# Kernel tuning notes

Hardware: AMD Instinct MI355X
Metric: run time of the kernel (lower is better)

Reference implementation:

```python
import jax, jax.numpy as jnp
import numpy as np

N_NODES = 100000
N_EDGES = 1600000
F_IN = 128
HID = 128
N_CLS = 40


def _glorot(key, shape):
    fan_in, fan_out = shape[0], shape[1]
    lim = (6.0 / (fan_in + fan_out)) ** 0.5
    return jax.random.uniform(key, shape, jnp.float32, -lim, lim)


def setup_inputs() -> dict:
    key = jax.random.key(0)
    ks = jax.random.split(key, 10)
    x = jax.random.normal(ks[0], (N_NODES, F_IN), jnp.float32)
    edge_index = jax.random.randint(ks[1], (2, N_EDGES), 0, N_NODES, jnp.int64)
    return {
        "x": x,
        "edge_index": edge_index,
        "W1l": _glorot(ks[2], (F_IN, HID)),   # applied to aggregated neighbors
        "W1r": _glorot(ks[3], (F_IN, HID)),   # applied to root features
        "b1": jnp.zeros((HID,), jnp.float32),
        "W2l": _glorot(ks[4], (HID, HID)),
        "W2r": _glorot(ks[5], (HID, HID)),
        "b2": jnp.zeros((HID,), jnp.float32),
        "Wout": _glorot(ks[6], (HID, N_CLS)),
        "bout": jnp.zeros((N_CLS,), jnp.float32),
    }


def _sage_conv(x, src, dst, Wl, Wr, b):
    # mean aggregation of neighbor messages x[src] at dst, then linear combine
    msgs = x[src]                                                   # [E, F] gather
    agg = jax.ops.segment_sum(msgs, dst, num_segments=N_NODES)      # [N, F]
    cnt = jax.ops.segment_sum(jnp.ones((src.shape[0],), x.dtype), dst,
                              num_segments=N_NODES)                 # [N]
    agg = agg / jnp.maximum(cnt, 1.0)[:, None]
    return agg @ Wl + x @ Wr + b


def reference(x, edge_index, W1l, W1r, b1, W2l, W2r, b2, Wout, bout):
    src, dst = edge_index[0], edge_index[1]
    h = jax.nn.relu(_sage_conv(x, src, dst, W1l, W1r, b1))
    # dropout is identity in deterministic (eval) reference
    h = jax.nn.relu(_sage_conv(h, src, dst, W2l, W2r, b2))
    return h @ Wout + bout
```

## Files before the change

### kernel.cpp

```cpp
#include <hip/hip_runtime.h>
#include <hip/hip_bf16.h>

#define N_NODES 100000
#define N_EDGES 1600000
#define FDIM 128
#define NCLS 40
#define NCLS_PAD 48

#define NBINS ((N_NODES + 255) / 256)
#define NBLKB 128
#define CHUNKB (N_EDGES / NBLKB)
#define SCANTOT (NBINS * NBLKB)
#define SCANB_NB ((SCANTOT + 1023) / 1024)

typedef __attribute__((ext_vector_type(8))) short short8;
typedef __attribute__((ext_vector_type(4))) float f32x4;

__device__ __forceinline__ float bf2f(unsigned short u) {
    union { unsigned int i; float f; } v; v.i = ((unsigned int)u) << 16; return v.f;
}
__device__ __forceinline__ unsigned short f2bf(float f) {
    __hip_bfloat16 h = __float2bfloat16(f);
    return *reinterpret_cast<unsigned short*>(&h);
}

__global__ void k_cvt_bf16(const float4* __restrict__ in, ushort4* __restrict__ out, int n4) {
    int i = blockIdx.x * blockDim.x + threadIdx.x;
    if (i >= n4) return;
    float4 v = in[i];
    ushort4 o;
    o.x = f2bf(v.x); o.y = f2bf(v.y); o.z = f2bf(v.z); o.w = f2bf(v.w);
    out[i] = o;
}

__global__ __launch_bounds__(256) void k_countB(const int* __restrict__ dst, int* __restrict__ bh) {
    __shared__ unsigned h[NBINS];
    for (int r = threadIdx.x; r < NBINS; r += 256) h[r] = 0u;
    __syncthreads();
    int base = blockIdx.x * CHUNKB;
    int end = base + CHUNKB; if (end > N_EDGES) end = N_EDGES;
    for (int e = base + threadIdx.x; e < end; e += 256)
        atomicAdd(&h[dst[e] >> 8], 1u);
    __syncthreads();
    for (int r = threadIdx.x; r < NBINS; r += 256)
        bh[blockIdx.x * NBINS + r] = (int)h[r];
}

__global__ __launch_bounds__(1024) void k_scanB1(const int* __restrict__ bh,
                                                 int* __restrict__ obh,
                                                 unsigned* __restrict__ bsumB) {
    __shared__ unsigned lds[1024];
    int t = threadIdx.x;
    int g = blockIdx.x * 1024 + t;
    unsigned v = 0u;
    int r = g >> 7, b = g & (NBLKB - 1);
    if (g < SCANTOT) v = (unsigned)bh[b * NBINS + r];
    lds[t] = v;
    __syncthreads();
    for (int d = 1; d < 1024; d <<= 1) {
        unsigned add = (t >= d) ? lds[t - d] : 0u;
        __syncthreads();
        lds[t] += add;
        __syncthreads();
    }
    if (g < SCANTOT) obh[b * NBINS + r] = (int)(lds[t] - v);
    if (t == 1023) bsumB[blockIdx.x] = lds[t];
}

__global__ void k_scanB2(const unsigned* __restrict__ bsumB, unsigned* __restrict__ boffB) {
    __shared__ unsigned lds[64];
    int t = threadIdx.x;
    unsigned v = (t < SCANB_NB) ? bsumB[t] : 0u;
    lds[t] = v;
    __syncthreads();
    for (int d = 1; d < 64; d <<= 1) {
        unsigned add = (t >= d) ? lds[t - d] : 0u;
        __syncthreads();
        lds[t] += add;
        __syncthreads();
    }
    if (t < SCANB_NB) boffB[t] = lds[t] - v;
}

__global__ __launch_bounds__(1024) void k_scanB3(int* __restrict__ obh,
                                                 const unsigned* __restrict__ boffB,
                                                 int* __restrict__ bucketbase) {
    int t = threadIdx.x;
    int g = blockIdx.x * 1024 + t;
    if (g < SCANTOT) {
        int r = g >> 7, b = g & (NBLKB - 1);
        int val = obh[b * NBINS + r] + (int)boffB[blockIdx.x];
        obh[b * NBINS + r] = val;
        if (b == 0) bucketbase[r] = val;
    }
    if (g == 0) bucketbase[NBINS] = N_EDGES;
}

__global__ __launch_bounds__(256) void k_binwriteB(const int* __restrict__ src, const int* __restrict__ dst,
                                                   const int* __restrict__ obh,
                                                   unsigned long long* __restrict__ bpack) {
    __shared__ unsigned pos[NBINS];
    for (int r = threadIdx.x; r < NBINS; r += 256)
        pos[r] = (unsigned)obh[blockIdx.x * NBINS + r];
    __syncthreads();
    int base = blockIdx.x * CHUNKB;
    int end = base + CHUNKB; if (end > N_EDGES) end = N_EDGES;
    for (int e = base + threadIdx.x; e < end; e += 256) {
        int d = dst[e];
        unsigned p = atomicAdd(&pos[d >> 8], 1u);
        bpack[p] = ((unsigned long long)(unsigned)d << 32) | (unsigned)src[e];
    }
}

__global__ __launch_bounds__(256) void k_bucket_csr(const unsigned long long* __restrict__ bpack,
                                                    const int* __restrict__ bucketbase,
                                                    int* __restrict__ rowptr,
                                                    int* __restrict__ esrc) {
    __shared__ unsigned c[256];
    int b = blockIdx.x;
    int t = threadIdx.x;
    int bb = bucketbase[b], be = bucketbase[b + 1];
    c[t] = 0u;
    __syncthreads();
    for (int i = bb + t; i < be; i += 256)
        atomicAdd(&c[(unsigned)(bpack[i] >> 32) & 255u], 1u);
    __syncthreads();
    unsigned own = c[t];
    for (int d = 1; d < 256; d <<= 1) {
        unsigned add = (t >= d) ? c[t - d] : 0u;
        __syncthreads();
        c[t] += add;
        __syncthreads();
    }
    unsigned excl = c[t] - own;
    int node = (b << 8) + t;
    if (node < N_NODES) rowptr[node] = bb + (int)excl;
    if (b == NBINS - 1 && t == 0) rowptr[N_NODES] = N_EDGES;
    __syncthreads();
    c[t] = excl;
    __syncthreads();
    for (int i = bb + t; i < be; i += 256) {
        unsigned long long p = bpack[i];
        unsigned slot = atomicAdd(&c[(unsigned)(p >> 32) & 255u], 1u);
        esrc[bb + (int)slot] = (int)(unsigned)p;
    }
}

__global__ void k_aggregate(const unsigned short* __restrict__ feat,
                            const int* __restrict__ esrc,
                            const int* __restrict__ rowptr,
                            unsigned short* __restrict__ out) {
    int node = blockIdx.x * 4 + (threadIdx.x >> 6);
    if (node >= N_NODES) return;
    int lane = threadIdx.x & 63;
    int sub = lane >> 4;
    int fl = lane & 15;
    int s = rowptr[node], e = rowptr[node + 1];
    float acc[8];
#pragma unroll
    for (int q = 0; q < 8; ++q) acc[q] = 0.f;

    for (int j = s + sub; j < e; j += 4) {
        int sv = esrc[j];
        short8 v = *(const short8*)(feat + (size_t)sv * FDIM + fl * 8);
#pragma unroll
        for (int q = 0; q < 8; ++q) acc[q] += bf2f((unsigned short)v[q]);
    }
#pragma unroll
    for (int q = 0; q < 8; ++q) {
        acc[q] += __shfl_xor(acc[q], 16, 64);
        acc[q] += __shfl_xor(acc[q], 32, 64);
    }
    int deg = e - s;
    float inv = 1.0f / (float)(deg > 1 ? deg : 1);
    if (sub == 0) {
        short8 o;
#pragma unroll
        for (int q = 0; q < 8; ++q) o[q] = (short)f2bf(acc[q] * inv);
        *(short8*)(out + (size_t)node * FDIM + fl * 8) = o;
    }
}

__global__ void k_pack(const float* __restrict__ Wl, const float* __restrict__ Wr,
                       const float* __restrict__ bin, unsigned short* __restrict__ Bp,
                       float* __restrict__ bout, int ncols_out, int ncols_src, int Keach) {
    int K = (Wr != nullptr) ? 2 * Keach : Keach;
    int idx = blockIdx.x * blockDim.x + threadIdx.x;
    if (idx >= ncols_out * K) return;
    int col = idx / K, k = idx % K;
    float v = 0.f;
    if (col < ncols_src)
        v = (k < Keach) ? Wl[(size_t)k * ncols_src + col]
                        : Wr[(size_t)(k - Keach) * ncols_src + col];
    Bp[((size_t)(k >> 3) * ncols_out + col) * 8 + (k & 7)] = f2bf(v);
    if (k == 0) bout[col] = (col < ncols_src) ? bin[col] : 0.f;
}

__global__ __launch_bounds__(256) void k_gemm_layer(
        const unsigned short* __restrict__ A0, const unsigned short* __restrict__ A1,
        const unsigned short* __restrict__ Bp, const float* __restrict__ bias,
        unsigned short* __restrict__ out) {
    int wave = threadIdx.x >> 6;
    int lane = threadIdx.x & 63;
    int rowblk = blockIdx.x * 64 + wave * 16;
    int lrow = lane & 15;
    int kgrp = lane >> 4;
    int arow = rowblk + lrow; if (arow > N_NODES - 1) arow = N_NODES - 1;

    f32x4 acc[8];
#pragma unroll
    for (int c = 0; c < 8; ++c) acc[c] = (f32x4){0.f, 0.f, 0.f, 0.f};

#pragma unroll
    for (int kb = 0; kb < 8; ++kb) {
        const unsigned short* Asrc = (kb < 4) ? A0 : A1;
        int kk = (kb & 3) * 32 + kgrp * 8;
        short8 a = *(const short8*)(Asrc + (size_t)arow * FDIM + kk);
        int k8 = kb * 4 + kgrp;
        const unsigned short* brow = Bp + ((size_t)k8 * FDIM + lrow) * 8;
#pragma unroll
        for (int c = 0; c < 8; ++c) {
            short8 b = *(const short8*)(brow + c * 16 * 8);
            acc[c] = __builtin_amdgcn_mfma_f32_16x16x32_bf16(a, b, acc[c], 0, 0, 0);
        }
    }

    int orowbase = rowblk + kgrp * 4;
#pragma unroll
    for (int c = 0; c < 8; ++c) {
        int col = c * 16 + lrow;
        float bv = bias[col];
#pragma unroll
        for (int i = 0; i < 4; ++i) {
            int r = orowbase + i;
            if (r < N_NODES) {
                float v = acc[c][i] + bv;
                v = fmaxf(v, 0.f);
                out[(size_t)r * FDIM + col] = f2bf(v);
            }
        }
    }
}

__global__ __launch_bounds__(256) void k_gemm_out(
        const unsigned short* __restrict__ A0, const unsigned short* __restrict__ Bp,
        const float* __restrict__ bias, float* __restrict__ out) {
    int wave = threadIdx.x >> 6;
    int lane = threadIdx.x & 63;
    int rowblk = blockIdx.x * 64 + wave * 16;
    int lrow = lane & 15;
    int kgrp = lane >> 4;
    int arow = rowblk + lrow; if (arow > N_NODES - 1) arow = N_NODES - 1;

    f32x4 acc[3];
#pragma unroll
    for (int c = 0; c < 3; ++c) acc[c] = (f32x4){0.f, 0.f, 0.f, 0.f};

#pragma unroll
    for (int kb = 0; kb < 4; ++kb) {
        int kk = kb * 32 + kgrp * 8;
        short8 a = *(const short8*)(A0 + (size_t)arow * FDIM + kk);
        int k8 = kb * 4 + kgrp;
        const unsigned short* brow = Bp + ((size_t)k8 * NCLS_PAD + lrow) * 8;
#pragma unroll
        for (int c = 0; c < 3; ++c) {
            short8 b = *(const short8*)(brow + c * 16 * 8);
            acc[c] = __builtin_amdgcn_mfma_f32_16x16x32_bf16(a, b, acc[c], 0, 0, 0);
        }
    }

    int orowbase = rowblk + kgrp * 4;
#pragma unroll
    for (int c = 0; c < 3; ++c) {
        int col = c * 16 + lrow;
        if (col < NCLS) {
            float bv = bias[col];
#pragma unroll
            for (int i = 0; i < 4; ++i) {
                int r = orowbase + i;
                if (r < N_NODES)
                    out[(size_t)r * NCLS + col] = acc[c][i] + bv;
            }
        }
    }
}

extern "C" void kernel_launch(void* const* d_in, const int* in_sizes, int n_in,
                              void* d_out, int out_size, void* d_ws, size_t ws_size,
                              hipStream_t stream) {
    const float* x    = (const float*)d_in[0];
    const int*   ei   = (const int*)d_in[1];
    const float* W1l  = (const float*)d_in[2];
    const float* W1r  = (const float*)d_in[3];
    const float* b1   = (const float*)d_in[4];
    const float* W2l  = (const float*)d_in[5];
    const float* W2r  = (const float*)d_in[6];
    const float* b2   = (const float*)d_in[7];
    const float* Wout = (const float*)d_in[8];
    const float* bout = (const float*)d_in[9];
    const int* src = ei;
    const int* dst = ei + N_EDGES;

    char* ws = (char*)d_ws;
    size_t off = 0;
    auto alloc = [&](size_t bytes) -> void* {
        void* p = ws + off;
        off += (bytes + 255) & ~(size_t)255;
        return p;
    };
    unsigned short* xb   = (unsigned short*)alloc((size_t)N_NODES * FDIM * 2);
    unsigned short* aggn = (unsigned short*)alloc((size_t)N_NODES * FDIM * 2);
    unsigned short* h1   = (unsigned short*)alloc((size_t)N_NODES * FDIM * 2);
    unsigned short* h2   = (unsigned short*)alloc((size_t)N_NODES * FDIM * 2);
    unsigned short* Bp1  = (unsigned short*)alloc((size_t)FDIM * 256 * 2);
    unsigned short* Bp2  = (unsigned short*)alloc((size_t)FDIM * 256 * 2);
    unsigned short* Bp3  = (unsigned short*)alloc((size_t)NCLS_PAD * FDIM * 2);
    float* b1p = (float*)alloc(FDIM * 4);
    float* b2p = (float*)alloc(FDIM * 4);
    float* b3p = (float*)alloc(NCLS_PAD * 4);
    int* rowptr    = (int*)alloc((size_t)(N_NODES + 1) * 4);
    int* esrc      = (int*)alloc((size_t)N_EDGES * 4);
    int* bh        = (int*)alloc((size_t)NBLKB * NBINS * 4);
    int* obh       = (int*)alloc((size_t)NBLKB * NBINS * 4);
    int* bucketbase= (int*)alloc((size_t)(NBINS + 1) * 4);
    unsigned* bsumB = (unsigned*)alloc((size_t)SCANB_NB * 4);
    unsigned* boffB = (unsigned*)alloc((size_t)SCANB_NB * 4);
    unsigned long long* bpack = (unsigned long long*)alloc((size_t)N_EDGES * 8);

    int n4 = N_NODES * FDIM / 4;
    k_cvt_bf16<<<(n4 + 255) / 256, 256, 0, stream>>>((const float4*)x, (ushort4*)xb, n4);

    k_pack<<<(FDIM * 256 + 255) / 256, 256, 0, stream>>>(W1l, W1r, b1, Bp1, b1p, FDIM, FDIM, FDIM);
    k_pack<<<(FDIM * 256 + 255) / 256, 256, 0, stream>>>(W2l, W2r, b2, Bp2, b2p, FDIM, FDIM, FDIM);
    k_pack<<<(NCLS_PAD * FDIM + 255) / 256, 256, 0, stream>>>(Wout, nullptr, bout, Bp3, b3p, NCLS_PAD, NCLS, FDIM);

    k_countB<<<NBLKB, 256, 0, stream>>>(dst, bh);
    k_scanB1<<<SCANB_NB, 1024, 0, stream>>>(bh, obh, bsumB);
    k_scanB2<<<1, 64, 0, stream>>>(bsumB, boffB);
    k_scanB3<<<SCANB_NB, 1024, 0, stream>>>(obh, boffB, bucketbase);
    k_binwriteB<<<NBLKB, 256, 0, stream>>>(src, dst, obh, bpack);
    k_bucket_csr<<<NBINS, 256, 0, stream>>>(bpack, bucketbase, rowptr, esrc);

    int aggGrid = (N_NODES + 3) / 4;
    int gemmGrid = (N_NODES + 63) / 64;

    k_aggregate<<<aggGrid, 256, 0, stream>>>(xb, esrc, rowptr, aggn);
    k_gemm_layer<<<gemmGrid, 256, 0, stream>>>(aggn, xb, Bp1, b1p, h1);
    k_aggregate<<<aggGrid, 256, 0, stream>>>(h1, esrc, rowptr, aggn);
    k_gemm_layer<<<gemmGrid, 256, 0, stream>>>(aggn, h1, Bp2, b2p, h2);
    k_gemm_out<<<gemmGrid, 256, 0, stream>>>(h2, Bp3, b3p, (float*)d_out);
}
```

Before: 293.1 us.

## Fuse neighbor aggregation into the layer GEMMs via LDS and merge the pack kernels

Each wave now gathers and mean-aggregates its 16 nodes into an LDS tile, then runs the MFMA GEMM directly from LDS. This removes the aggn intermediate round-trip through global memory. The second layer also keeps its ReLU output in LDS and applies the output projection in the same kernel, removing the h2 buffer. The three weight-pack launches are merged into one. The tradeoff is less gather parallelism: there are now 1563 blocks, each looping serially over 16 nodes per wave, instead of 25000 small blocks. That can reduce latency hiding for the irregular gathers.

```diff
diff --git a/kernel.cpp b/kernel.cpp
--- a/kernel.cpp
+++ b/kernel.cpp
@@ -12,6 +12,8 @@
 #define CHUNKB (N_EDGES / NBLKB)
 #define SCANTOT (NBINS * NBLKB)
 #define SCANB_NB ((SCANTOT + 1023) / 1024)
+
+#define LPAD 136
 
 typedef __attribute__((ext_vector_type(8))) short short8;
 typedef __attribute__((ext_vector_type(4))) float f32x4;
@@ -146,47 +148,10 @@
     }
 }
 
-__global__ void k_aggregate(const unsigned short* __restrict__ feat,
-                            const int* __restrict__ esrc,
-                            const int* __restrict__ rowptr,
-                            unsigned short* __restrict__ out) {
-    int node = blockIdx.x * 4 + (threadIdx.x >> 6);
-    if (node >= N_NODES) return;
-    int lane = threadIdx.x & 63;
-    int sub = lane >> 4;
-    int fl = lane & 15;
-    int s = rowptr[node], e = rowptr[node + 1];
-    float acc[8];
-#pragma unroll
-    for (int q = 0; q < 8; ++q) acc[q] = 0.f;
-
-    for (int j = s + sub; j < e; j += 4) {
-        int sv = esrc[j];
-        short8 v = *(const short8*)(feat + (size_t)sv * FDIM + fl * 8);
-#pragma unroll
-        for (int q = 0; q < 8; ++q) acc[q] += bf2f((unsigned short)v[q]);
-    }
-#pragma unroll
-    for (int q = 0; q < 8; ++q) {
-        acc[q] += __shfl_xor(acc[q], 16, 64);
-        acc[q] += __shfl_xor(acc[q], 32, 64);
-    }
-    int deg = e - s;
-    float inv = 1.0f / (float)(deg > 1 ? deg : 1);
-    if (sub == 0) {
-        short8 o;
-#pragma unroll
-        for (int q = 0; q < 8; ++q) o[q] = (short)f2bf(acc[q] * inv);
-        *(short8*)(out + (size_t)node * FDIM + fl * 8) = o;
-    }
-}
-
-__global__ void k_pack(const float* __restrict__ Wl, const float* __restrict__ Wr,
-                       const float* __restrict__ bin, unsigned short* __restrict__ Bp,
-                       float* __restrict__ bout, int ncols_out, int ncols_src, int Keach) {
+__device__ __forceinline__ void pack_one(const float* Wl, const float* Wr, const float* bin,
+                                         unsigned short* Bp, float* bout,
+                                         int ncols_out, int ncols_src, int Keach, int idx) {
     int K = (Wr != nullptr) ? 2 * Keach : Keach;
-    int idx = blockIdx.x * blockDim.x + threadIdx.x;
-    if (idx >= ncols_out * K) return;
     int col = idx / K, k = idx % K;
     float v = 0.f;
     if (col < ncols_src)
@@ -196,36 +161,84 @@
     if (k == 0) bout[col] = (col < ncols_src) ? bin[col] : 0.f;
 }
 
-__global__ __launch_bounds__(256) void k_gemm_layer(
-        const unsigned short* __restrict__ A0, const unsigned short* __restrict__ A1,
+#define PACK1 (FDIM * 256)
+#define PACK2 (FDIM * 256)
+#define PACK3 (NCLS_PAD * FDIM)
+__global__ void k_pack_all(const float* __restrict__ W1l, const float* __restrict__ W1r,
+                           const float* __restrict__ b1, unsigned short* __restrict__ Bp1, float* __restrict__ b1p,
+                           const float* __restrict__ W2l, const float* __restrict__ W2r,
+                           const float* __restrict__ b2, unsigned short* __restrict__ Bp2, float* __restrict__ b2p,
+                           const float* __restrict__ Wout, const float* __restrict__ bo,
+                           unsigned short* __restrict__ Bp3, float* __restrict__ b3p) {
+    int idx = blockIdx.x * blockDim.x + threadIdx.x;
+    if (idx < PACK1) { pack_one(W1l, W1r, b1, Bp1, b1p, FDIM, FDIM, FDIM, idx); return; }
+    idx -= PACK1;
+    if (idx < PACK2) { pack_one(W2l, W2r, b2, Bp2, b2p, FDIM, FDIM, FDIM, idx); return; }
+    idx -= PACK2;
+    if (idx < PACK3) { pack_one(Wout, nullptr, bo, Bp3, b3p, NCLS_PAD, NCLS, FDIM, idx); }
+}
+
+__global__ __launch_bounds__(256) void k_fused_layer(
+        const unsigned short* __restrict__ feat,
+        const int* __restrict__ esrc, const int* __restrict__ rowptr,
         const unsigned short* __restrict__ Bp, const float* __restrict__ bias,
         unsigned short* __restrict__ out) {
-    int wave = threadIdx.x >> 6;
-    int lane = threadIdx.x & 63;
-    int rowblk = blockIdx.x * 64 + wave * 16;
-    int lrow = lane & 15;
-    int kgrp = lane >> 4;
-    int arow = rowblk + lrow; if (arow > N_NODES - 1) arow = N_NODES - 1;
-
-    f32x4 acc[8];
-#pragma unroll
-    for (int c = 0; c < 8; ++c) acc[c] = (f32x4){0.f, 0.f, 0.f, 0.f};
+    __shared__ unsigned short Alds[4][16][LPAD];
+    int wave = threadIdx.x >> 6, lane = threadIdx.x & 63;
+    int sub = lane >> 4, fl = lane & 15;
+    int wbase = blockIdx.x * 64 + wave * 16;
+
+    for (int n = 0; n < 16; ++n) {
+        int node = wbase + n;
+        float acc[8];
+#pragma unroll
+        for (int q = 0; q < 8; ++q) acc[q] = 0.f;
+        int deg = 0;
+        if (node < N_NODES) {
+            int s = rowptr[node], e = rowptr[node + 1];
+            deg = e - s;
+            for (int j = s + sub; j < e; j += 4) {
+                int sv = esrc[j];
+                short8 v = *(const short8*)(feat + (size_t)sv * FDIM + fl * 8);
+#pragma unroll
+                for (int q = 0; q < 8; ++q) acc[q] += bf2f((unsigned short)v[q]);
+            }
+        }
+#pragma unroll
+        for (int q = 0; q < 8; ++q) {
+            acc[q] += __shfl_xor(acc[q], 16, 64);
+            acc[q] += __shfl_xor(acc[q], 32, 64);
+        }
+        if (sub == 0) {
+            float inv = 1.0f / (float)(deg > 1 ? deg : 1);
+            short8 o;
+#pragma unroll
+            for (int q = 0; q < 8; ++q) o[q] = (short)f2bf(acc[q] * inv);
+            *(short8*)(&Alds[wave][n][fl * 8]) = o;
+        }
+    }
+
+    int lrow = lane & 15, kgrp = lane >> 4;
+    int arow = wbase + lrow; if (arow > N_NODES - 1) arow = N_NODES - 1;
+    f32x4 acc2[8];
+#pragma unroll
+    for (int c = 0; c < 8; ++c) acc2[c] = (f32x4){0.f, 0.f, 0.f, 0.f};
 
 #pragma unroll
     for (int kb = 0; kb < 8; ++kb) {
-        const unsigned short* Asrc = (kb < 4) ? A0 : A1;
-        int kk = (kb & 3) * 32 + kgrp * 8;
-        short8 a = *(const short8*)(Asrc + (size_t)arow * FDIM + kk);
+        short8 a;
+        if (kb < 4) a = *(const short8*)(&Alds[wave][lrow][kb * 32 + kgrp * 8]);
+        else        a = *(const short8*)(feat + (size_t)arow * FDIM + (kb - 4) * 32 + kgrp * 8);
         int k8 = kb * 4 + kgrp;
         const unsigned short* brow = Bp + ((size_t)k8 * FDIM + lrow) * 8;
 #pragma unroll
         for (int c = 0; c < 8; ++c) {
             short8 b = *(const short8*)(brow + c * 16 * 8);
-            acc[c] = __builtin_amdgcn_mfma_f32_16x16x32_bf16(a, b, acc[c], 0, 0, 0);
-        }
-    }
-
-    int orowbase = rowblk + kgrp * 4;
+            acc2[c] = __builtin_amdgcn_mfma_f32_16x16x32_bf16(a, b, acc2[c], 0, 0, 0);
+        }
+    }
+
+    int orowbase = wbase + kgrp * 4;
 #pragma unroll
     for (int c = 0; c < 8; ++c) {
         int col = c * 16 + lrow;
@@ -234,7 +247,7 @@
         for (int i = 0; i < 4; ++i) {
             int r = orowbase + i;
             if (r < N_NODES) {
-                float v = acc[c][i] + bv;
+                float v = acc2[c][i] + bv;
                 v = fmaxf(v, 0.f);
                 out[(size_t)r * FDIM + col] = f2bf(v);
             }
@@ -242,44 +255,107 @@
     }
 }
 
-__global__ __launch_bounds__(256) void k_gemm_out(
-        const unsigned short* __restrict__ A0, const unsigned short* __restrict__ Bp,
-        const float* __restrict__ bias, float* __restrict__ out) {
-    int wave = threadIdx.x >> 6;
-    int lane = threadIdx.x & 63;
-    int rowblk = blockIdx.x * 64 + wave * 16;
-    int lrow = lane & 15;
-    int kgrp = lane >> 4;
-    int arow = rowblk + lrow; if (arow > N_NODES - 1) arow = N_NODES - 1;
-
-    f32x4 acc[3];
-#pragma unroll
-    for (int c = 0; c < 3; ++c) acc[c] = (f32x4){0.f, 0.f, 0.f, 0.f};
+__global__ __launch_bounds__(256) void k_fused_final(
+        const unsigned short* __restrict__ feat,
+        const int* __restrict__ esrc, const int* __restrict__ rowptr,
+        const unsigned short* __restrict__ Bp, const float* __restrict__ bias,
+        const unsigned short* __restrict__ Bp3, const float* __restrict__ bias3,
+        float* __restrict__ out) {
+    __shared__ unsigned short Alds[4][16][LPAD];
+    int wave = threadIdx.x >> 6, lane = threadIdx.x & 63;
+    int sub = lane >> 4, fl = lane & 15;
+    int wbase = blockIdx.x * 64 + wave * 16;
+
+    for (int n = 0; n < 16; ++n) {
+        int node = wbase + n;
+        float acc[8];
+#pragma unroll
+        for (int q = 0; q < 8; ++q) acc[q] = 0.f;
+        int deg = 0;
+        if (node < N_NODES) {
+            int s = rowptr[node], e = rowptr[node + 1];
+            deg = e - s;
+            for (int j = s + sub; j < e; j += 4) {
+                int sv = esrc[j];
+                short8 v = *(const short8*)(feat + (size_t)sv * FDIM + fl * 8);
+#pragma unroll
+                for (int q = 0; q < 8; ++q) acc[q] += bf2f((unsigned short)v[q]);
+            }
+        }
+#pragma unroll
+        for (int q = 0; q < 8; ++q) {
+            acc[q] += __shfl_xor(acc[q], 16, 64);
+            acc[q] += __shfl_xor(acc[q], 32, 64);
+        }
+        if (sub == 0) {
+            float inv = 1.0f / (float)(deg > 1 ? deg : 1);
+            short8 o;
+#pragma unroll
+            for (int q = 0; q < 8; ++q) o[q] = (short)f2bf(acc[q] * inv);
+            *(short8*)(&Alds[wave][n][fl * 8]) = o;
+        }
+    }
+
+    int lrow = lane & 15, kgrp = lane >> 4;
+    int arow = wbase + lrow; if (arow > N_NODES - 1) arow = N_NODES - 1;
+    f32x4 acc2[8];
+#pragma unroll
+    for (int c = 0; c < 8; ++c) acc2[c] = (f32x4){0.f, 0.f, 0.f, 0.f};
+
+#pragma unroll
+    for (int kb = 0; kb < 8; ++kb) {
+        short8 a;
+        if (kb < 4) a = *(const short8*)(&Alds[wave][lrow][kb * 32 + kgrp * 8]);
+        else        a = *(const short8*)(feat + (size_t)arow * FDIM + (kb - 4) * 32 + kgrp * 8);
+        int k8 = kb * 4 + kgrp;
+        const unsigned short* brow = Bp + ((size_t)k8 * FDIM + lrow) * 8;
+#pragma unroll
+        for (int c = 0; c < 8; ++c) {
+            short8 b = *(const short8*)(brow + c * 16 * 8);
+            acc2[c] = __builtin_amdgcn_mfma_f32_16x16x32_bf16(a, b, acc2[c], 0, 0, 0);
+        }
+    }
+
+    int srowbase = kgrp * 4;
+#pragma unroll
+    for (int c = 0; c < 8; ++c) {
+        int col = c * 16 + lrow;
+        float bv = bias[col];
+#pragma unroll
+        for (int i = 0; i < 4; ++i) {
+            float v = acc2[c][i] + bv;
+            v = fmaxf(v, 0.f);
+            Alds[wave][srowbase + i][col] = f2bf(v);
+        }
+    }
+
+    f32x4 acc3[3];
+#pragma unroll
+    for (int c = 0; c < 3; ++c) acc3[c] = (f32x4){0.f, 0.f, 0.f, 0.f};
 
 #pragma unroll
     for (int kb = 0; kb < 4; ++kb) {
-        int kk = kb * 32 + kgrp * 8;
-        short8 a = *(const short8*)(A0 + (size_t)arow * FDIM + kk);
+        short8 a = *(const short8*)(&Alds[wave][lrow][kb * 32 + kgrp * 8]);
         int k8 = kb * 4 + kgrp;
-        const unsigned short* brow = Bp + ((size_t)k8 * NCLS_PAD + lrow) * 8;
+        const unsigned short* brow = Bp3 + ((size_t)k8 * NCLS_PAD + lrow) * 8;
 #pragma unroll
         for (int c = 0; c < 3; ++c) {
             short8 b = *(const short8*)(brow + c * 16 * 8);
-            acc[c] = __builtin_amdgcn_mfma_f32_16x16x32_bf16(a, b, acc[c], 0, 0, 0);
-        }
-    }
-
-    int orowbase = rowblk + kgrp * 4;
+            acc3[c] = __builtin_amdgcn_mfma_f32_16x16x32_bf16(a, b, acc3[c], 0, 0, 0);
+        }
+    }
+
+    int orowbase = wbase + kgrp * 4;
 #pragma unroll
     for (int c = 0; c < 3; ++c) {
         int col = c * 16 + lrow;
         if (col < NCLS) {
-            float bv = bias[col];
+            float bv = bias3[col];
 #pragma unroll
             for (int i = 0; i < 4; ++i) {
                 int r = orowbase + i;
                 if (r < N_NODES)
-                    out[(size_t)r * NCLS + col] = acc[c][i] + bv;
+                    out[(size_t)r * NCLS + col] = acc3[c][i] + bv;
             }
         }
     }
@@ -309,9 +385,7 @@
         return p;
     };
     unsigned short* xb   = (unsigned short*)alloc((size_t)N_NODES * FDIM * 2);
-    unsigned short* aggn = (unsigned short*)alloc((size_t)N_NODES * FDIM * 2);
     unsigned short* h1   = (unsigned short*)alloc((size_t)N_NODES * FDIM * 2);
-    unsigned short* h2   = (unsigned short*)alloc((size_t)N_NODES * FDIM * 2);
     unsigned short* Bp1  = (unsigned short*)alloc((size_t)FDIM * 256 * 2);
     unsigned short* Bp2  = (unsigned short*)alloc((size_t)FDIM * 256 * 2);
     unsigned short* Bp3  = (unsigned short*)alloc((size_t)NCLS_PAD * FDIM * 2);
@@ -330,9 +404,9 @@
     int n4 = N_NODES * FDIM / 4;
     k_cvt_bf16<<<(n4 + 255) / 256, 256, 0, stream>>>((const float4*)x, (ushort4*)xb, n4);
 
-    k_pack<<<(FDIM * 256 + 255) / 256, 256, 0, stream>>>(W1l, W1r, b1, Bp1, b1p, FDIM, FDIM, FDIM);
-    k_pack<<<(FDIM * 256 + 255) / 256, 256, 0, stream>>>(W2l, W2r, b2, Bp2, b2p, FDIM, FDIM, FDIM);
-    k_pack<<<(NCLS_PAD * FDIM + 255) / 256, 256, 0, stream>>>(Wout, nullptr, bout, Bp3, b3p, NCLS_PAD, NCLS, FDIM);
+    int packTot = PACK1 + PACK2 + PACK3;
+    k_pack_all<<<(packTot + 255) / 256, 256, 0, stream>>>(
+        W1l, W1r, b1, Bp1, b1p, W2l, W2r, b2, Bp2, b2p, Wout, bout, Bp3, b3p);
 
     k_countB<<<NBLKB, 256, 0, stream>>>(dst, bh);
     k_scanB1<<<SCANB_NB, 1024, 0, stream>>>(bh, obh, bsumB);
@@ -341,12 +415,8 @@
     k_binwriteB<<<NBLKB, 256, 0, stream>>>(src, dst, obh, bpack);
     k_bucket_csr<<<NBINS, 256, 0, stream>>>(bpack, bucketbase, rowptr, esrc);
 
-    int aggGrid = (N_NODES + 3) / 4;
-    int gemmGrid = (N_NODES + 63) / 64;
-
-    k_aggregate<<<aggGrid, 256, 0, stream>>>(xb, esrc, rowptr, aggn);
-    k_gemm_layer<<<gemmGrid, 256, 0, stream>>>(aggn, xb, Bp1, b1p, h1);
-    k_aggregate<<<aggGrid, 256, 0, stream>>>(h1, esrc, rowptr, aggn);
-    k_gemm_layer<<<gemmGrid, 256, 0, stream>>>(aggn, h1, Bp2, b2p, h2);
-    k_gemm_out<<<gemmGrid, 256, 0, stream>>>(h2, Bp3, b3p, (float*)d_out);
-}
+    int fusedGrid = (N_NODES + 63) / 64;
+
+    k_fused_layer<<<fusedGrid, 256, 0, stream>>>(xb, esrc, rowptr, Bp1, b1p, h1);
+    k_fused_final<<<fusedGrid, 256, 0, stream>>>(h1, esrc, rowptr, Bp2, b2p, Bp3, b3p, (float*)d_out);
+}
```

New measurement: 353.3 us. 1.21x slower.

## Fuse prologue kernels, merge scan passes, fuse layer-2 GEMM with output GEMM

Applied to the files above, without the earlier changes.

Combines the edge-count, bf16 conversion and weight-pack kernels into one prologue launch with block-range dispatch. It folds the small block-offset scan into the final scan pass. It also fuses the second SAGE layer GEMM with the classifier GEMM by staging the ReLU'd bf16 tile in LDS per wave. This avoids writing and re-reading the h2 intermediate and cuts several launches. The cost is more LDS use and some redundant serial scan work per block.

```diff
diff --git a/kernel.cpp b/kernel.cpp
--- a/kernel.cpp
+++ b/kernel.cpp
@@ -13,6 +13,16 @@
 #define SCANTOT (NBINS * NBLKB)
 #define SCANB_NB ((SCANTOT + 1023) / 1024)
 
+#define LPAD 136
+
+#define PACK1 (FDIM * 256)
+#define PACK2 (FDIM * 256)
+#define PACK3 (NCLS_PAD * FDIM)
+#define PACKTOT (PACK1 + PACK2 + PACK3)
+#define PACK_NB ((PACKTOT + 255) / 256)
+#define CVT_N4 (N_NODES * FDIM / 4)
+#define CVT_NB ((CVT_N4 + 255) / 256)
+
 typedef __attribute__((ext_vector_type(8))) short short8;
 typedef __attribute__((ext_vector_type(4))) float f32x4;
 
@@ -24,26 +34,60 @@
     return *reinterpret_cast<unsigned short*>(&h);
 }
 
-__global__ void k_cvt_bf16(const float4* __restrict__ in, ushort4* __restrict__ out, int n4) {
-    int i = blockIdx.x * blockDim.x + threadIdx.x;
-    if (i >= n4) return;
-    float4 v = in[i];
-    ushort4 o;
-    o.x = f2bf(v.x); o.y = f2bf(v.y); o.z = f2bf(v.z); o.w = f2bf(v.w);
-    out[i] = o;
-}
-
-__global__ __launch_bounds__(256) void k_countB(const int* __restrict__ dst, int* __restrict__ bh) {
+__device__ __forceinline__ void pack_one(const float* Wl, const float* Wr, const float* bin,
+                                         unsigned short* Bp, float* bout,
+                                         int ncols_out, int ncols_src, int Keach, int idx) {
+    int K = (Wr != nullptr) ? 2 * Keach : Keach;
+    int col = idx / K, k = idx % K;
+    float v = 0.f;
+    if (col < ncols_src)
+        v = (k < Keach) ? Wl[(size_t)k * ncols_src + col]
+                        : Wr[(size_t)(k - Keach) * ncols_src + col];
+    Bp[((size_t)(k >> 3) * ncols_out + col) * 8 + (k & 7)] = f2bf(v);
+    if (k == 0) bout[col] = (col < ncols_src) ? bin[col] : 0.f;
+}
+
+__global__ __launch_bounds__(256) void k_prologue(
+        const int* __restrict__ dst, int* __restrict__ bh,
+        const float4* __restrict__ x4, ushort4* __restrict__ xb4,
+        const float* __restrict__ W1l, const float* __restrict__ W1r,
+        const float* __restrict__ b1, unsigned short* __restrict__ Bp1, float* __restrict__ b1p,
+        const float* __restrict__ W2l, const float* __restrict__ W2r,
+        const float* __restrict__ b2, unsigned short* __restrict__ Bp2, float* __restrict__ b2p,
+        const float* __restrict__ Wout, const float* __restrict__ bo,
+        unsigned short* __restrict__ Bp3, float* __restrict__ b3p) {
     __shared__ unsigned h[NBINS];
-    for (int r = threadIdx.x; r < NBINS; r += 256) h[r] = 0u;
-    __syncthreads();
-    int base = blockIdx.x * CHUNKB;
-    int end = base + CHUNKB; if (end > N_EDGES) end = N_EDGES;
-    for (int e = base + threadIdx.x; e < end; e += 256)
-        atomicAdd(&h[dst[e] >> 8], 1u);
-    __syncthreads();
-    for (int r = threadIdx.x; r < NBINS; r += 256)
-        bh[blockIdx.x * NBINS + r] = (int)h[r];
+    int b = blockIdx.x;
+    if (b < NBLKB) {
+        for (int r = threadIdx.x; r < NBINS; r += 256) h[r] = 0u;
+        __syncthreads();
+        int base = b * CHUNKB;
+        int end = base + CHUNKB; if (end > N_EDGES) end = N_EDGES;
+        for (int e = base + threadIdx.x; e < end; e += 256)
+            atomicAdd(&h[dst[e] >> 8], 1u);
+        __syncthreads();
+        for (int r = threadIdx.x; r < NBINS; r += 256)
+            bh[b * NBINS + r] = (int)h[r];
+        return;
+    }
+    b -= NBLKB;
+    if (b < CVT_NB) {
+        int i = b * 256 + threadIdx.x;
+        if (i < CVT_N4) {
+            float4 v = x4[i];
+            ushort4 o;
+            o.x = f2bf(v.x); o.y = f2bf(v.y); o.z = f2bf(v.z); o.w = f2bf(v.w);
+            xb4[i] = o;
+        }
+        return;
+    }
+    b -= CVT_NB;
+    int idx = b * 256 + threadIdx.x;
+    if (idx < PACK1) { pack_one(W1l, W1r, b1, Bp1, b1p, FDIM, FDIM, FDIM, idx); return; }
+    idx -= PACK1;
+    if (idx < PACK2) { pack_one(W2l, W2r, b2, Bp2, b2p, FDIM, FDIM, FDIM, idx); return; }
+    idx -= PACK2;
+    if (idx < PACK3) { pack_one(Wout, nullptr, bo, Bp3, b3p, NCLS_PAD, NCLS, FDIM, idx); }
 }
 
 __global__ __launch_bounds__(1024) void k_scanB1(const int* __restrict__ bh,
@@ -67,29 +111,22 @@
     if (t == 1023) bsumB[blockIdx.x] = lds[t];
 }
 
-__global__ void k_scanB2(const unsigned* __restrict__ bsumB, unsigned* __restrict__ boffB) {
-    __shared__ unsigned lds[64];
+__global__ __launch_bounds__(1024) void k_scanB3(int* __restrict__ obh,
+                                                 const unsigned* __restrict__ bsumB,
+                                                 int* __restrict__ bucketbase) {
+    __shared__ unsigned soff[SCANB_NB];
     int t = threadIdx.x;
-    unsigned v = (t < SCANB_NB) ? bsumB[t] : 0u;
-    lds[t] = v;
-    __syncthreads();
-    for (int d = 1; d < 64; d <<= 1) {
-        unsigned add = (t >= d) ? lds[t - d] : 0u;
-        __syncthreads();
-        lds[t] += add;
-        __syncthreads();
-    }
-    if (t < SCANB_NB) boffB[t] = lds[t] - v;
-}
-
-__global__ __launch_bounds__(1024) void k_scanB3(int* __restrict__ obh,
-                                                 const unsigned* __restrict__ boffB,
-                                                 int* __restrict__ bucketbase) {
-    int t = threadIdx.x;
+    if (t < SCANB_NB) soff[t] = bsumB[t];
+    __syncthreads();
+    if (t == 0) {
+        unsigned run = 0;
+        for (int i = 0; i < SCANB_NB; ++i) { unsigned v = soff[i]; soff[i] = run; run += v; }
+    }
+    __syncthreads();
     int g = blockIdx.x * 1024 + t;
     if (g < SCANTOT) {
         int r = g >> 7, b = g & (NBLKB - 1);
-        int val = obh[b * NBINS + r] + (int)boffB[blockIdx.x];
+        int val = obh[b * NBINS + r] + (int)soff[blockIdx.x];
         obh[b * NBINS + r] = val;
         if (b == 0) bucketbase[r] = val;
     }
@@ -181,21 +218,6 @@
     }
 }
 
-__global__ void k_pack(const float* __restrict__ Wl, const float* __restrict__ Wr,
-                       const float* __restrict__ bin, unsigned short* __restrict__ Bp,
-                       float* __restrict__ bout, int ncols_out, int ncols_src, int Keach) {
-    int K = (Wr != nullptr) ? 2 * Keach : Keach;
-    int idx = blockIdx.x * blockDim.x + threadIdx.x;
-    if (idx >= ncols_out * K) return;
-    int col = idx / K, k = idx % K;
-    float v = 0.f;
-    if (col < ncols_src)
-        v = (k < Keach) ? Wl[(size_t)k * ncols_src + col]
-                        : Wr[(size_t)(k - Keach) * ncols_src + col];
-    Bp[((size_t)(k >> 3) * ncols_out + col) * 8 + (k & 7)] = f2bf(v);
-    if (k == 0) bout[col] = (col < ncols_src) ? bin[col] : 0.f;
-}
-
 __global__ __launch_bounds__(256) void k_gemm_layer(
         const unsigned short* __restrict__ A0, const unsigned short* __restrict__ A1,
         const unsigned short* __restrict__ Bp, const float* __restrict__ bias,
@@ -242,9 +264,12 @@
     }
 }
 
-__global__ __launch_bounds__(256) void k_gemm_out(
-        const unsigned short* __restrict__ A0, const unsigned short* __restrict__ Bp,
-        const float* __restrict__ bias, float* __restrict__ out) {
+__global__ __launch_bounds__(256) void k_gemm_final(
+        const unsigned short* __restrict__ A0, const unsigned short* __restrict__ A1,
+        const unsigned short* __restrict__ Bp, const float* __restrict__ bias,
+        const unsigned short* __restrict__ Bp3, const float* __restrict__ bias3,
+        float* __restrict__ out) {
+    __shared__ unsigned short Alds[4][16][LPAD];
     int wave = threadIdx.x >> 6;
     int lane = threadIdx.x & 63;
     int rowblk = blockIdx.x * 64 + wave * 16;
@@ -252,20 +277,50 @@
     int kgrp = lane >> 4;
     int arow = rowblk + lrow; if (arow > N_NODES - 1) arow = N_NODES - 1;
 
-    f32x4 acc[3];
-#pragma unroll
-    for (int c = 0; c < 3; ++c) acc[c] = (f32x4){0.f, 0.f, 0.f, 0.f};
+    f32x4 acc2[8];
+#pragma unroll
+    for (int c = 0; c < 8; ++c) acc2[c] = (f32x4){0.f, 0.f, 0.f, 0.f};
+
+#pragma unroll
+    for (int kb = 0; kb < 8; ++kb) {
+        const unsigned short* Asrc = (kb < 4) ? A0 : A1;
+        int kk = (kb & 3) * 32 + kgrp * 8;
+        short8 a = *(const short8*)(Asrc + (size_t)arow * FDIM + kk);
+        int k8 = kb * 4 + kgrp;
+        const unsigned short* brow = Bp + ((size_t)k8 * FDIM + lrow) * 8;
+#pragma unroll
+        for (int c = 0; c < 8; ++c) {
+            short8 b = *(const short8*)(brow + c * 16 * 8);
+            acc2[c] = __builtin_amdgcn_mfma_f32_16x16x32_bf16(a, b, acc2[c], 0, 0, 0);
+        }
+    }
+
+    int srowbase = kgrp * 4;
+#pragma unroll
+    for (int c = 0; c < 8; ++c) {
+        int col = c * 16 + lrow;
+        float bv = bias[col];
+#pragma unroll
+        for (int i = 0; i < 4; ++i) {
+            float v = acc2[c][i] + bv;
+            v = fmaxf(v, 0.f);
+            Alds[wave][srowbase + i][col] = f2bf(v);
+        }
+    }
+
+    f32x4 acc3[3];
+#pragma unroll
+    for (int c = 0; c < 3; ++c) acc3[c] = (f32x4){0.f, 0.f, 0.f, 0.f};
 
 #pragma unroll
     for (int kb = 0; kb < 4; ++kb) {
-        int kk = kb * 32 + kgrp * 8;
-        short8 a = *(const short8*)(A0 + (size_t)arow * FDIM + kk);
+        short8 a = *(const short8*)(&Alds[wave][lrow][kb * 32 + kgrp * 8]);
         int k8 = kb * 4 + kgrp;
-        const unsigned short* brow = Bp + ((size_t)k8 * NCLS_PAD + lrow) * 8;
+        const unsigned short* brow = Bp3 + ((size_t)k8 * NCLS_PAD + lrow) * 8;
 #pragma unroll
         for (int c = 0; c < 3; ++c) {
             short8 b = *(const short8*)(brow + c * 16 * 8);
-            acc[c] = __builtin_amdgcn_mfma_f32_16x16x32_bf16(a, b, acc[c], 0, 0, 0);
+            acc3[c] = __builtin_amdgcn_mfma_f32_16x16x32_bf16(a, b, acc3[c], 0, 0, 0);
         }
     }
 
@@ -274,12 +329,12 @@
     for (int c = 0; c < 3; ++c) {
         int col = c * 16 + lrow;
         if (col < NCLS) {
-            float bv = bias[col];
+            float bv = bias3[col];
 #pragma unroll
             for (int i = 0; i < 4; ++i) {
                 int r = orowbase + i;
                 if (r < N_NODES)
-                    out[(size_t)r * NCLS + col] = acc[c][i] + bv;
+                    out[(size_t)r * NCLS + col] = acc3[c][i] + bv;
             }
         }
     }
@@ -311,7 +366,6 @@
     unsigned short* xb   = (unsigned short*)alloc((size_t)N_NODES * FDIM * 2);
     unsigned short* aggn = (unsigned short*)alloc((size_t)N_NODES * FDIM * 2);
     unsigned short* h1   = (unsigned short*)alloc((size_t)N_NODES * FDIM * 2);
-    unsigned short* h2   = (unsigned short*)alloc((size_t)N_NODES * FDIM * 2);
     unsigned short* Bp1  = (unsigned short*)alloc((size_t)FDIM * 256 * 2);
     unsigned short* Bp2  = (unsigned short*)alloc((size_t)FDIM * 256 * 2);
     unsigned short* Bp3  = (unsigned short*)alloc((size_t)NCLS_PAD * FDIM * 2);
@@ -324,20 +378,15 @@
     int* obh       = (int*)alloc((size_t)NBLKB * NBINS * 4);
     int* bucketbase= (int*)alloc((size_t)(NBINS + 1) * 4);
     unsigned* bsumB = (unsigned*)alloc((size_t)SCANB_NB * 4);
-    unsigned* boffB = (unsigned*)alloc((size_t)SCANB_NB * 4);
     unsigned long long* bpack = (unsigned long long*)alloc((size_t)N_EDGES * 8);
 
-    int n4 = N_NODES * FDIM / 4;
-    k_cvt_bf16<<<(n4 + 255) / 256, 256, 0, stream>>>((const float4*)x, (ushort4*)xb, n4);
-
-    k_pack<<<(FDIM * 256 + 255) / 256, 256, 0, stream>>>(W1l, W1r, b1, Bp1, b1p, FDIM, FDIM, FDIM);
-    k_pack<<<(FDIM * 256 + 255) / 256, 256, 0, stream>>>(W2l, W2r, b2, Bp2, b2p, FDIM, FDIM, FDIM);
-    k_pack<<<(NCLS_PAD * FDIM + 255) / 256, 256, 0, stream>>>(Wout, nullptr, bout, Bp3, b3p, NCLS_PAD, NCLS, FDIM);
-
-    k_countB<<<NBLKB, 256, 0, stream>>>(dst, bh);
+    int proGrid = NBLKB + CVT_NB + PACK_NB;
+    k_prologue<<<proGrid, 256, 0, stream>>>(
+        dst, bh, (const float4*)x, (ushort4*)xb,
+        W1l, W1r, b1, Bp1, b1p, W2l, W2r, b2, Bp2, b2p, Wout, bout, Bp3, b3p);
+
     k_scanB1<<<SCANB_NB, 1024, 0, stream>>>(bh, obh, bsumB);
-    k_scanB2<<<1, 64, 0, stream>>>(bsumB, boffB);
-    k_scanB3<<<SCANB_NB, 1024, 0, stream>>>(obh, boffB, bucketbase);
+    k_scanB3<<<SCANB_NB, 1024, 0, stream>>>(obh, bsumB, bucketbase);
     k_binwriteB<<<NBLKB, 256, 0, stream>>>(src, dst, obh, bpack);
     k_bucket_csr<<<NBINS, 256, 0, stream>>>(bpack, bucketbase, rowptr, esrc);
 
@@ -347,6 +396,5 @@
     k_aggregate<<<aggGrid, 256, 0, stream>>>(xb, esrc, rowptr, aggn);
     k_gemm_layer<<<gemmGrid, 256, 0, stream>>>(aggn, xb, Bp1, b1p, h1);
     k_aggregate<<<aggGrid, 256, 0, stream>>>(h1, esrc, rowptr, aggn);
-    k_gemm_layer<<<gemmGrid, 256, 0, stream>>>(aggn, h1, Bp2, b2p, h2);
-    k_gemm_out<<<gemmGrid, 256, 0, stream>>>(h2, Bp3, b3p, (float*)d_out);
-}
+    k_gemm_final<<<gemmGrid, 256, 0, stream>>>(aggn, h1, Bp2, b2p, Bp3, b3p, (float*)d_out);
+}
```

Measured after the change: 266.0 us. 9.2% less time.
